# Kernel optimization log

Measured on AMD Instinct MI355X. Metric: run time of the kernel, lower is better.

Reference implementation:

```python
import jax, jax.numpy as jnp
import numpy as np

B, N, D = 4, 4096, 1024
H, DH = 16, 64            # heads, dim_head; inner = H*DH = 1024
FF = 4 * D                # ffn inner dim
EPS = 1e-5


def setup_inputs() -> dict:
    key = jax.random.key(0)
    ks = jax.random.split(key, 8)
    s = 0.02
    return {
        "x": jax.random.normal(ks[0], (B, N, D), jnp.float32),
        "W_qkv": jax.random.normal(ks[1], (D, 3 * H * DH), jnp.float32) * s,
        "W_out": jax.random.normal(ks[2], (H * DH, D), jnp.float32) * s,
        "b_out": jnp.zeros((D,), jnp.float32),
        "ln_g": jnp.ones((D,), jnp.float32),
        "ln_b": jnp.zeros((D,), jnp.float32),
        "W1": jax.random.normal(ks[3], (D, FF), jnp.float32) * s,
        "b1": jnp.zeros((FF,), jnp.float32),
        "W2": jax.random.normal(ks[4], (FF, D), jnp.float32) * s,
        "b2": jnp.zeros((D,), jnp.float32),
    }


def reference(x, W_qkv, W_out, b_out, ln_g, ln_b, W1, b1, W2, b2):
    b, n, _ = x.shape
    scale = DH ** -0.5

    # --- LinearAttention (dual-softmax kernelized attention) ---
    qkv = x @ W_qkv                                   # [b, n, 3*H*DH]
    q, k, v = jnp.split(qkv, 3, axis=-1)
    split = lambda t: t.reshape(b, n, H, DH).transpose(0, 2, 1, 3)  # [b, h, n, d]
    q = jax.nn.softmax(split(q) * scale, axis=-1)     # softmax over head dim
    k = jax.nn.softmax(split(k), axis=-2)             # softmax over sequence
    v = split(v)
    context = jnp.einsum('bhnd,bhne->bhde', q, k)     # [b, h, d, e] -- linear in n
    out = jnp.einsum('bhde,bhnd->bhne', context, v)   # [b, h, n, e]
    out = out.transpose(0, 2, 1, 3).reshape(b, n, H * DH)
    attn = out @ W_out + b_out                        # to_out (dropout=0 at eval)

    # --- LayerNorm ---
    mu = jnp.mean(attn, axis=-1, keepdims=True)
    var = jnp.var(attn, axis=-1, keepdims=True)
    h = (attn - mu) * jax.lax.rsqrt(var + EPS) * ln_g + ln_b

    # --- FeedForward: Linear -> SiLU -> Linear ---
    y = jax.nn.silu(h @ W1 + b1) @ W2 + b2
    return y
```

## Files before the change

### kernel.cpp

```cpp
#include <hip/hip_runtime.h>
#include <hip/hip_bf16.h>

typedef __bf16 bf16x8 __attribute__((ext_vector_type(8)));
typedef __bf16 bf16x4 __attribute__((ext_vector_type(4)));
typedef float  f32x4  __attribute__((ext_vector_type(4)));

#define GLOAD_LDS16(gp, lp) \
  __builtin_amdgcn_global_load_lds((const __attribute__((address_space(1))) void*)(gp), \
                                   (__attribute__((address_space(3))) void*)(lp), 16, 0, 0)


__global__ __launch_bounds__(256) void zero_f32(float* __restrict__ p, int n) {
  int i = (blockIdx.x * 256 + threadIdx.x) * 4;
  if (i < n) *(float4*)(p + i) = make_float4(0.f, 0.f, 0.f, 0.f);
}

__global__ __launch_bounds__(256) void cvt_f32_bf16(const float* __restrict__ in,
                                                    __bf16* __restrict__ out, long n) {
  long i = ((long)blockIdx.x * 256 + threadIdx.x) * 4;
  if (i >= n) return;
  float4 v = *(const float4*)(in + i);
  bf16x4 o;
  o[0] = (__bf16)v.x; o[1] = (__bf16)v.y; o[2] = (__bf16)v.z; o[3] = (__bf16)v.w;
  *(bf16x4*)(out + i) = o;
}

__global__ __launch_bounds__(256) void cvt_wT(const float* __restrict__ W,
                                              __bf16* __restrict__ WT, int K, int N) {
  __shared__ float t[32][33];
  int k0 = blockIdx.x * 32, n0 = blockIdx.y * 32;
  int tx = threadIdx.x, ty = threadIdx.y;
  #pragma unroll
  for (int i = 0; i < 32; i += 8)
    t[ty + i][tx] = W[(size_t)(k0 + ty + i) * N + n0 + tx];
  __syncthreads();
  #pragma unroll
  for (int i = 0; i < 32; i += 8)
    WT[(size_t)(n0 + ty + i) * K + k0 + tx] = (__bf16)t[tx][ty + i];
}


enum { EPI_BF16 = 0, EPI_F32_BIAS = 1, EPI_BF16_SILU = 2, EPI_BF16_BIAS = 3 };

template <int EPI>
__global__ __launch_bounds__(512, 1)
void gemm256(const __bf16* __restrict__ A, const __bf16* __restrict__ B,
             void* __restrict__ Cout, const float* __restrict__ bias,
             int M, int N, int K) {
  __shared__ __bf16 lds[4 * 16384];
  const int tid = threadIdx.x;
  const int w = tid >> 6, l = tid & 63;
  const int brow = blockIdx.x * 256;
  const int bcol = blockIdx.y * 256;
  const int wr = w >> 2, wc = w & 3;
  const int lr = l & 15, lk = (l >> 4) * 8;
  const int rdo = ((lk >> 3) ^ ((lr >> 1) & 3)) << 3;
  const int NT = K >> 5;

  const int rr = w * 16 + (l >> 2);
  const int oct = l & 3;
  const int soct = oct ^ ((rr >> 1) & 3);
  const __bf16* gA0 = A + (size_t)(brow + rr) * K + soct * 8;
  const __bf16* gA1 = A + (size_t)(brow + 128 + rr) * K + soct * 8;
  const __bf16* gB0 = B + (size_t)(bcol + rr) * K + soct * 8;
  const __bf16* gB1 = B + (size_t)(bcol + 128 + rr) * K + soct * 8;
  __bf16* const ldsw = lds + w * 512;

  f32x4 acc[8][4] = {};

  auto stage = [&](int buf) {
    __bf16* d = ldsw + buf * 16384;
    GLOAD_LDS16(gA0, d);
    GLOAD_LDS16(gA1, d + 4096);
    GLOAD_LDS16(gB0, d + 8192);
    GLOAD_LDS16(gB1, d + 12288);
    gA0 += 32; gA1 += 32; gB0 += 32; gB1 += 32;
  };

  stage(0); stage(1); stage(2);

  const int abase = (wr * 128 + lr) * 32 + rdo;
  const int bbase = 8192 + (wc * 64 + lr) * 32 + rdo;

  for (int t = 0; t < NT; ++t) {
    if (t + 2 < NT)      asm volatile("s_waitcnt vmcnt(8)" ::: "memory");
    else if (t + 1 < NT) asm volatile("s_waitcnt vmcnt(4)" ::: "memory");
    else                 asm volatile("s_waitcnt vmcnt(0)" ::: "memory");
    __builtin_amdgcn_s_barrier();
    if (t + 3 < NT) stage((t + 3) & 3);

    const __bf16* sA = lds + (t & 3) * 16384 + abase;
    const __bf16* sB = lds + (t & 3) * 16384 + bbase;

    bf16x8 bfr[4], afr[4];
    #pragma unroll
    for (int n = 0; n < 4; ++n)
      bfr[n] = *(const bf16x8*)(sB + n * 512);
    #pragma unroll
    for (int m = 0; m < 4; ++m)
      afr[m] = *(const bf16x8*)(sA + m * 512);

    __builtin_amdgcn_s_setprio(1);
    #pragma unroll
    for (int m = 0; m < 4; ++m)
      #pragma unroll
      for (int n = 0; n < 4; ++n)
        acc[m][n] = __builtin_amdgcn_mfma_f32_16x16x32_bf16(afr[m], bfr[n], acc[m][n], 0, 0, 0);
    __builtin_amdgcn_s_setprio(0);

    #pragma unroll
    for (int m = 0; m < 4; ++m)
      afr[m] = *(const bf16x8*)(sA + (m + 4) * 512);

    __builtin_amdgcn_s_setprio(1);
    #pragma unroll
    for (int m = 0; m < 4; ++m)
      #pragma unroll
      for (int n = 0; n < 4; ++n)
        acc[m + 4][n] = __builtin_amdgcn_mfma_f32_16x16x32_bf16(afr[m], bfr[n], acc[m + 4][n], 0, 0, 0);
    __builtin_amdgcn_s_setprio(0);
  }

  #pragma unroll
  for (int m = 0; m < 8; ++m) {
    int row0 = brow + wr * 128 + m * 16 + (l >> 4) * 4;
    #pragma unroll
    for (int n = 0; n < 4; ++n) {
      int col = bcol + wc * 64 + n * 16 + lr;
      float bv = (EPI == EPI_BF16) ? 0.f : bias[col];
      #pragma unroll
      for (int j = 0; j < 4; ++j) {
        float v = acc[m][n][j];
        size_t off = (size_t)(row0 + j) * N + col;
        if (EPI == EPI_BF16) {
          ((__bf16*)Cout)[off] = (__bf16)v;
        } else if (EPI == EPI_F32_BIAS) {
          ((float*)Cout)[off] = v + bv;
        } else if (EPI == EPI_BF16_BIAS) {
          ((__bf16*)Cout)[off] = (__bf16)(v + bv);
        } else {
          float z = v + bv;
          ((__bf16*)Cout)[off] = (__bf16)(z / (1.f + __expf(-z)));
        }
      }
    }
  }
}


__global__ __launch_bounds__(256) void q_softmax(__bf16* __restrict__ qkv) {
  qkv += (size_t)blockIdx.z * 4096 * 3072;
  int wg = blockIdx.x * 4 + (threadIdx.x >> 6);
  int l = threadIdx.x & 63;
  int row = wg >> 4, h = wg & 15;
  __bf16* p = qkv + (size_t)row * 3072 + h * 64 + l;
  float v = (float)*p * 0.125f;
  float m = v;
  #pragma unroll
  for (int s = 32; s; s >>= 1) m = fmaxf(m, __shfl_xor(m, s));
  float e = __expf(v - m);
  float sum = e;
  #pragma unroll
  for (int s = 32; s; s >>= 1) sum += __shfl_xor(sum, s);
  *p = (__bf16)(e / sum);
}

__global__ __launch_bounds__(256) void k_exp(__bf16* __restrict__ qkv, float* __restrict__ S) {
  qkv += (size_t)blockIdx.z * 4096 * 3072;
  S   += (size_t)blockIdx.z * 1024;
  int c = blockIdx.x * 256 + threadIdx.x;
  int n0 = blockIdx.y * 128;
  float sum = 0.f;
  __bf16* base = qkv + (size_t)n0 * 3072 + 1024 + c;
  for (int i = 0; i < 128; ++i) {
    __bf16* p = base + (size_t)i * 3072;
    float e = __expf((float)*p);
    __bf16 eb = (__bf16)e;
    *p = eb;
    sum += (float)eb;
  }
  atomicAdd(&S[c], sum);
}

__global__ __launch_bounds__(256) void ctx_gemm(const __bf16* __restrict__ qkv,
                                                float* __restrict__ ctx) {
  qkv += (size_t)blockIdx.z * 4096 * 3072;
  ctx += (size_t)blockIdx.z * 16 * 4096;
  int h = blockIdx.x;
  int k0base = blockIdx.y * 1024;
  __shared__ __bf16 sQ[64 * 32];
  __shared__ __bf16 sK[64 * 32];
  int tid = threadIdx.x, w = tid >> 6, l = tid & 63;
  int lr = l & 15, lk = (l >> 4) * 8;
  int srow = tid >> 3, scol = (tid & 7) * 8;
  f32x4 acc[4] = {};

  for (int kc = 0; kc < 1024; kc += 32) {
    size_t grow = (size_t)(k0base + kc + srow) * 3072;
    bf16x8 qv = *(const bf16x8*)(qkv + grow + h * 64 + scol);
    bf16x8 kv = *(const bf16x8*)(qkv + grow + 1024 + h * 64 + scol);
    __syncthreads();
    #pragma unroll
    for (int j = 0; j < 8; ++j) {
      sQ[(scol + j) * 32 + srow] = qv[j];
      sK[(scol + j) * 32 + srow] = kv[j];
    }
    __syncthreads();
    bf16x8 a = *(const bf16x8*)(sQ + (w * 16 + lr) * 32 + lk);
    #pragma unroll
    for (int n = 0; n < 4; ++n) {
      bf16x8 bb = *(const bf16x8*)(sK + (n * 16 + lr) * 32 + lk);
      acc[n] = __builtin_amdgcn_mfma_f32_16x16x32_bf16(a, bb, acc[n], 0, 0, 0);
    }
  }
  float* cbase = ctx + (size_t)h * 64 * 64;
  #pragma unroll
  for (int n = 0; n < 4; ++n) {
    int col = n * 16 + lr;
    #pragma unroll
    for (int j = 0; j < 4; ++j) {
      int row = w * 16 + (l >> 4) * 4 + j;
      atomicAdd(cbase + row * 64 + col, acc[n][j]);
    }
  }
}

__global__ __launch_bounds__(256) void pv_gemm(const __bf16* __restrict__ qkv,
                                               const float* __restrict__ ctx,
                                               const float* __restrict__ S,
                                               __bf16* __restrict__ outpv) {
  qkv   += (size_t)blockIdx.z * 4096 * 3072;
  ctx   += (size_t)blockIdx.z * 16 * 4096;
  S     += (size_t)blockIdx.z * 1024;
  outpv += (size_t)blockIdx.z * 4096 * 1024;
  int h = blockIdx.y;
  int row0 = blockIdx.x * 128;
  __shared__ __bf16 sC[64 * 64];
  int tid = threadIdx.x;
  const float* cb = ctx + (size_t)h * 4096;
  for (int i = tid; i < 4096; i += 256) {
    int d = i >> 6, e = i & 63;
    sC[e * 64 + d] = (__bf16)cb[i];
  }
  __syncthreads();
  int w = tid >> 6, l = tid & 63;
  int lr = l & 15, lk = (l >> 4) * 8;
  f32x4 acc[2][4] = {};
  const __bf16* vbase = qkv + 2048 + h * 64;
  #pragma unroll
  for (int kk = 0; kk < 64; kk += 32) {
    #pragma unroll
    for (int m = 0; m < 2; ++m) {
      int r = row0 + w * 32 + m * 16 + lr;
      bf16x8 a = *(const bf16x8*)(vbase + (size_t)r * 3072 + kk + lk);
      #pragma unroll
      for (int n = 0; n < 4; ++n) {
        bf16x8 bb = *(const bf16x8*)(sC + (n * 16 + lr) * 64 + kk + lk);
        acc[m][n] = __builtin_amdgcn_mfma_f32_16x16x32_bf16(a, bb, acc[m][n], 0, 0, 0);
      }
    }
  }
  #pragma unroll
  for (int m = 0; m < 2; ++m) {
    int rb = row0 + w * 32 + m * 16 + (l >> 4) * 4;
    #pragma unroll
    for (int n = 0; n < 4; ++n) {
      int e = n * 16 + lr;
      float inv = 1.0f / S[h * 64 + e];
      #pragma unroll
      for (int j = 0; j < 4; ++j)
        outpv[(size_t)(rb + j) * 1024 + h * 64 + e] = (__bf16)(acc[m][n][j] * inv);
    }
  }
}

__global__ __launch_bounds__(256) void layernorm_k(const __bf16* __restrict__ attn,
                                                   const float* __restrict__ g,
                                                   const float* __restrict__ beta,
                                                   __bf16* __restrict__ out) {
  int row = blockIdx.x;
  int t = threadIdx.x;
  bf16x4 v4 = *(const bf16x4*)(attn + (size_t)row * 1024 + t * 4);
  float v0 = (float)v4[0], v1 = (float)v4[1], v2 = (float)v4[2], v3 = (float)v4[3];
  float s = v0 + v1 + v2 + v3;
  float ss = v0 * v0 + v1 * v1 + v2 * v2 + v3 * v3;
  #pragma unroll
  for (int sh = 32; sh; sh >>= 1) { s += __shfl_xor(s, sh); ss += __shfl_xor(ss, sh); }
  __shared__ float red[8];
  int w = t >> 6, l = t & 63;
  if (l == 0) { red[w] = s; red[4 + w] = ss; }
  __syncthreads();
  s = red[0] + red[1] + red[2] + red[3];
  ss = red[4] + red[5] + red[6] + red[7];
  float mu = s * (1.f / 1024.f);
  float var = ss * (1.f / 1024.f) - mu * mu;
  float rstd = rsqrtf(var + 1e-5f);
  float4 gg = *(const float4*)(g + t * 4);
  float4 bb = *(const float4*)(beta + t * 4);
  bf16x4 o;
  o[0] = (__bf16)((v0 - mu) * rstd * gg.x + bb.x);
  o[1] = (__bf16)((v1 - mu) * rstd * gg.y + bb.y);
  o[2] = (__bf16)((v2 - mu) * rstd * gg.z + bb.z);
  o[3] = (__bf16)((v3 - mu) * rstd * gg.w + bb.w);
  *(bf16x4*)(out + (size_t)row * 1024 + t * 4) = o;
}


extern "C" void kernel_launch(void* const* d_in, const int* in_sizes, int n_in,
                              void* d_out, int out_size, void* d_ws, size_t ws_size,
                              hipStream_t stream) {
  const float* x     = (const float*)d_in[0];
  const float* W_qkv = (const float*)d_in[1];
  const float* W_out = (const float*)d_in[2];
  const float* b_out = (const float*)d_in[3];
  const float* ln_g  = (const float*)d_in[4];
  const float* ln_b  = (const float*)d_in[5];
  const float* W1    = (const float*)d_in[6];
  const float* b1    = (const float*)d_in[7];
  const float* W2    = (const float*)d_in[8];
  const float* b2    = (const float*)d_in[9];

  char* ws = (char*)d_ws;
  size_t off = 0;
  auto alloc = [&](size_t bytes) { void* p = ws + off; off += (bytes + 255) & ~(size_t)255; return p; };

  __bf16* wqkvT = (__bf16*)alloc(3072ull * 1024 * 2);
  __bf16* woutT = (__bf16*)alloc(1024ull * 1024 * 2);
  __bf16* w1T   = (__bf16*)alloc(4096ull * 1024 * 2);
  __bf16* w2T   = (__bf16*)alloc(1024ull * 4096 * 2);

  cvt_wT<<<dim3(32, 96), dim3(32, 8), 0, stream>>>(W_qkv, wqkvT, 1024, 3072);
  cvt_wT<<<dim3(32, 32), dim3(32, 8), 0, stream>>>(W_out, woutT, 1024, 1024);
  cvt_wT<<<dim3(32, 128), dim3(32, 8), 0, stream>>>(W1, w1T, 1024, 4096);
  cvt_wT<<<dim3(128, 32), dim3(32, 8), 0, stream>>>(W2, w2T, 4096, 1024);

  const size_t FULL_NEED = 196ull << 20;

  if (ws_size >= FULL_NEED) {
    float*  Sctx  = (float*)alloc((4096ull + 4 * 16 * 4096) * 4);
    __bf16* xb    = (__bf16*)alloc(16384ull * 1024 * 2);
    __bf16* qkv   = (__bf16*)alloc(16384ull * 3072 * 2);
    __bf16* outpv = (__bf16*)alloc(16384ull * 1024 * 2);

    float* S   = Sctx;
    float* ctx = Sctx + 4096;
    __bf16* attn = (__bf16*)((char*)qkv + (64ull << 20));
    __bf16* hln  = xb;
    __bf16* ffn1 = qkv;

    cvt_f32_bf16<<<16384, 256, 0, stream>>>(x, xb, 16777216L);
    zero_f32<<<260, 256, 0, stream>>>(Sctx, 266240);

    gemm256<EPI_BF16><<<dim3(64, 12), 512, 0, stream>>>(xb, wqkvT, qkv, nullptr, 16384, 3072, 1024);
    q_softmax<<<dim3(16384, 1, 4), 256, 0, stream>>>(qkv);
    k_exp<<<dim3(4, 32, 4), 256, 0, stream>>>(qkv, S);
    ctx_gemm<<<dim3(16, 4, 4), 256, 0, stream>>>(qkv, ctx);
    pv_gemm<<<dim3(32, 16, 4), 256, 0, stream>>>(qkv, ctx, S, outpv);

    gemm256<EPI_BF16_BIAS><<<dim3(64, 4), 512, 0, stream>>>(outpv, woutT, attn, b_out, 16384, 1024, 1024);
    layernorm_k<<<16384, 256, 0, stream>>>(attn, ln_g, ln_b, hln);
    gemm256<EPI_BF16_SILU><<<dim3(64, 16), 512, 0, stream>>>(hln, w1T, ffn1, b1, 16384, 4096, 1024);
    gemm256<EPI_F32_BIAS><<<dim3(64, 4), 512, 0, stream>>>(ffn1, w2T, (float*)d_out, b2, 16384, 1024, 4096);
  } else {
    float*  Sctx  = (float*)alloc(66560ull * 4);
    __bf16* xb    = (__bf16*)alloc(16384ull * 1024 * 2);
    __bf16* outpv = (__bf16*)alloc(16384ull * 1024 * 2);
    __bf16* qkv_b = (__bf16*)alloc(4096ull * 3072 * 2);

    float* S   = Sctx;
    float* ctx = Sctx + 1024;
    __bf16* attn = xb;
    __bf16* hln  = outpv;
    __bf16* fchunk = xb;

    cvt_f32_bf16<<<16384, 256, 0, stream>>>(x, xb, 16777216L);

    for (int b = 0; b < 4; ++b) {
      const __bf16* xb_b = xb + (size_t)b * 4096 * 1024;
      gemm256<EPI_BF16><<<dim3(16, 12), 512, 0, stream>>>(xb_b, wqkvT, qkv_b, nullptr, 4096, 3072, 1024);
      zero_f32<<<65, 256, 0, stream>>>(Sctx, 66560);
      q_softmax<<<dim3(16384, 1, 1), 256, 0, stream>>>(qkv_b);
      k_exp<<<dim3(4, 32, 1), 256, 0, stream>>>(qkv_b, S);
      ctx_gemm<<<dim3(16, 4, 1), 256, 0, stream>>>(qkv_b, ctx);
      pv_gemm<<<dim3(32, 16, 1), 256, 0, stream>>>(qkv_b, ctx, S, outpv + (size_t)b * 4096 * 1024);
    }

    gemm256<EPI_BF16_BIAS><<<dim3(64, 4), 512, 0, stream>>>(outpv, woutT, attn, b_out, 16384, 1024, 1024);
    layernorm_k<<<16384, 256, 0, stream>>>(attn, ln_g, ln_b, hln);

    for (int c = 0; c < 4; ++c) {
      const __bf16* h_c = hln + (size_t)c * 4096 * 1024;
      float* out_c = (float*)d_out + (size_t)c * 4096 * 1024;
      gemm256<EPI_BF16_SILU><<<dim3(16, 16), 512, 0, stream>>>(h_c, w1T, fchunk, b1, 4096, 4096, 1024);
      gemm256<EPI_F32_BIAS><<<dim3(16, 4), 512, 0, stream>>>(fchunk, w2T, out_c, b2, 4096, 1024, 4096);
    }
  }
}
```

Before: 587.5 us.

## Restructure GEMM main loop into 64-wide K tiles with interleaved half-stage prefetch

Replaces the 4-buffer, 32-wide-K ring in the 256x256 GEMM with two 64-wide K buffers, each split into two 32-wide halves. Each iteration runs four sub-phases, and each sub-phase issues the prefetch for one A or B half between its LDS reads and its MFMA block. It adds explicit lgkmcnt waits with scheduling barriers. The aim is to spread global-to-LDS traffic evenly across the MFMA work and cut the number of full barrier-wait points per K element. The cost is more barriers per iteration and tighter hand-managed vmcnt accounting, which is fragile.

```diff
diff --git a/kernel.cpp b/kernel.cpp
--- a/kernel.cpp
+++ b/kernel.cpp
@@ -8,6 +8,8 @@
 #define GLOAD_LDS16(gp, lp) \
   __builtin_amdgcn_global_load_lds((const __attribute__((address_space(1))) void*)(gp), \
                                    (__attribute__((address_space(3))) void*)(lp), 16, 0, 0)
+#define LGKM0 do { asm volatile("s_waitcnt lgkmcnt(0)" ::: "memory"); \
+                   __builtin_amdgcn_sched_barrier(0); } while (0)
 
 
 __global__ __launch_bounds__(256) void zero_f32(float* __restrict__ p, int n) {
@@ -47,78 +49,123 @@
 void gemm256(const __bf16* __restrict__ A, const __bf16* __restrict__ B,
              void* __restrict__ Cout, const float* __restrict__ bias,
              int M, int N, int K) {
-  __shared__ __bf16 lds[4 * 16384];
+  __shared__ __bf16 lds[65536];
   const int tid = threadIdx.x;
   const int w = tid >> 6, l = tid & 63;
   const int brow = blockIdx.x * 256;
   const int bcol = blockIdx.y * 256;
   const int wr = w >> 2, wc = w & 3;
-  const int lr = l & 15, lk = (l >> 4) * 8;
-  const int rdo = ((lk >> 3) ^ ((lr >> 1) & 3)) << 3;
-  const int NT = K >> 5;
-
-  const int rr = w * 16 + (l >> 2);
-  const int oct = l & 3;
-  const int soct = oct ^ ((rr >> 1) & 3);
-  const __bf16* gA0 = A + (size_t)(brow + rr) * K + soct * 8;
-  const __bf16* gA1 = A + (size_t)(brow + 128 + rr) * K + soct * 8;
-  const __bf16* gB0 = B + (size_t)(bcol + rr) * K + soct * 8;
-  const __bf16* gB1 = B + (size_t)(bcol + 128 + rr) * K + soct * 8;
-  __bf16* const ldsw = lds + w * 512;
+  const int lr = l & 15;
+  const int rdo8 = ((l >> 4) ^ ((lr >> 1) & 3)) << 3;
+  const int NT = K >> 6;
+
+  const int aoff = (wr * 128 + lr) * 32 + rdo8;
+  const int boff = 16384 + (wc * 64 + lr) * 32 + rdo8;
+
+  const int srow = w * 16 + (l >> 2);
+  const int soct8 = ((l & 3) ^ ((l >> 3) & 3)) * 8;
+  const __bf16* pA0 = A + (size_t)(brow + srow) * K + soct8;
+  const __bf16* pA1 = A + (size_t)(brow + 128 + srow) * K + soct8;
+  const __bf16* pB0 = B + (size_t)(bcol + srow) * K + soct8;
+  const __bf16* pB1 = B + (size_t)(bcol + 128 + srow) * K + soct8;
+
+  auto stageA = [&](int k, int Tt) {
+    size_t cofs = (size_t)Tt * 64 + k * 32;
+    __bf16* d = lds + (Tt & 1) * 32768 + k * 8192 + w * 512;
+    GLOAD_LDS16(pA0 + cofs, d);
+    GLOAD_LDS16(pA1 + cofs, d + 4096);
+  };
+  auto stageB = [&](int k, int Tt) {
+    size_t cofs = (size_t)Tt * 64 + k * 32;
+    __bf16* d = lds + (Tt & 1) * 32768 + 16384 + k * 8192 + w * 512;
+    GLOAD_LDS16(pB0 + cofs, d);
+    GLOAD_LDS16(pB1 + cofs, d + 4096);
+  };
 
   f32x4 acc[8][4] = {};
-
-  auto stage = [&](int buf) {
-    __bf16* d = ldsw + buf * 16384;
-    GLOAD_LDS16(gA0, d);
-    GLOAD_LDS16(gA1, d + 4096);
-    GLOAD_LDS16(gB0, d + 8192);
-    GLOAD_LDS16(gB1, d + 12288);
-    gA0 += 32; gA1 += 32; gB0 += 32; gB1 += 32;
-  };
-
-  stage(0); stage(1); stage(2);
-
-  const int abase = (wr * 128 + lr) * 32 + rdo;
-  const int bbase = 8192 + (wc * 64 + lr) * 32 + rdo;
-
-  for (int t = 0; t < NT; ++t) {
-    if (t + 2 < NT)      asm volatile("s_waitcnt vmcnt(8)" ::: "memory");
-    else if (t + 1 < NT) asm volatile("s_waitcnt vmcnt(4)" ::: "memory");
-    else                 asm volatile("s_waitcnt vmcnt(0)" ::: "memory");
+  bf16x8 afr[4], bfr[4];
+
+  stageA(0, 0); stageB(0, 0);
+  stageA(1, 0); stageB(1, 0);
+  stageA(0, 1); stageB(0, 1);
+
+  for (int T = 0; T < NT; ++T) {
+    const int buf = (T & 1) * 32768;
+    const bool s1 = (T + 1 < NT), s2 = (T + 2 < NT);
+
+    if (s1) asm volatile("s_waitcnt vmcnt(8)" ::: "memory");
+    else    asm volatile("s_waitcnt vmcnt(4)" ::: "memory");
     __builtin_amdgcn_s_barrier();
-    if (t + 3 < NT) stage((t + 3) & 3);
-
-    const __bf16* sA = lds + (t & 3) * 16384 + abase;
-    const __bf16* sB = lds + (t & 3) * 16384 + bbase;
-
-    bf16x8 bfr[4], afr[4];
-    #pragma unroll
-    for (int n = 0; n < 4; ++n)
-      bfr[n] = *(const bf16x8*)(sB + n * 512);
-    #pragma unroll
-    for (int m = 0; m < 4; ++m)
-      afr[m] = *(const bf16x8*)(sA + m * 512);
-
-    __builtin_amdgcn_s_setprio(1);
-    #pragma unroll
-    for (int m = 0; m < 4; ++m)
-      #pragma unroll
-      for (int n = 0; n < 4; ++n)
-        acc[m][n] = __builtin_amdgcn_mfma_f32_16x16x32_bf16(afr[m], bfr[n], acc[m][n], 0, 0, 0);
-    __builtin_amdgcn_s_setprio(0);
-
-    #pragma unroll
-    for (int m = 0; m < 4; ++m)
-      afr[m] = *(const bf16x8*)(sA + (m + 4) * 512);
-
-    __builtin_amdgcn_s_setprio(1);
-    #pragma unroll
-    for (int m = 0; m < 4; ++m)
-      #pragma unroll
-      for (int n = 0; n < 4; ++n)
-        acc[m + 4][n] = __builtin_amdgcn_mfma_f32_16x16x32_bf16(afr[m], bfr[n], acc[m + 4][n], 0, 0, 0);
-    __builtin_amdgcn_s_setprio(0);
+    {
+      const __bf16* pb = lds + buf + boff;
+      const __bf16* pa = lds + buf + aoff;
+      #pragma unroll
+      for (int n = 0; n < 4; ++n) bfr[n] = *(const bf16x8*)(pb + n * 512);
+      #pragma unroll
+      for (int m = 0; m < 4; ++m) afr[m] = *(const bf16x8*)(pa + m * 512);
+      if (s1) stageA(1, T + 1);
+      LGKM0;
+      __builtin_amdgcn_s_setprio(1);
+      #pragma unroll
+      for (int m = 0; m < 4; ++m)
+        #pragma unroll
+        for (int n = 0; n < 4; ++n)
+          acc[m][n] = __builtin_amdgcn_mfma_f32_16x16x32_bf16(afr[m], bfr[n], acc[m][n], 0, 0, 0);
+      __builtin_amdgcn_s_setprio(0);
+    }
+
+    __builtin_amdgcn_s_barrier();
+    {
+      const __bf16* pa = lds + buf + aoff + 2048;
+      #pragma unroll
+      for (int m = 0; m < 4; ++m) afr[m] = *(const bf16x8*)(pa + m * 512);
+      if (s1) stageB(1, T + 1);
+      LGKM0;
+      __builtin_amdgcn_s_setprio(1);
+      #pragma unroll
+      for (int m = 0; m < 4; ++m)
+        #pragma unroll
+        for (int n = 0; n < 4; ++n)
+          acc[m + 4][n] = __builtin_amdgcn_mfma_f32_16x16x32_bf16(afr[m], bfr[n], acc[m + 4][n], 0, 0, 0);
+      __builtin_amdgcn_s_setprio(0);
+    }
+
+    if (s1) asm volatile("s_waitcnt vmcnt(8)" ::: "memory");
+    else    asm volatile("s_waitcnt vmcnt(0)" ::: "memory");
+    __builtin_amdgcn_s_barrier();
+    {
+      const __bf16* pb = lds + buf + 8192 + boff;
+      const __bf16* pa = lds + buf + 8192 + aoff;
+      #pragma unroll
+      for (int n = 0; n < 4; ++n) bfr[n] = *(const bf16x8*)(pb + n * 512);
+      #pragma unroll
+      for (int m = 0; m < 4; ++m) afr[m] = *(const bf16x8*)(pa + m * 512);
+      if (s2) stageA(0, T + 2);
+      LGKM0;
+      __builtin_amdgcn_s_setprio(1);
+      #pragma unroll
+      for (int m = 0; m < 4; ++m)
+        #pragma unroll
+        for (int n = 0; n < 4; ++n)
+          acc[m][n] = __builtin_amdgcn_mfma_f32_16x16x32_bf16(afr[m], bfr[n], acc[m][n], 0, 0, 0);
+      __builtin_amdgcn_s_setprio(0);
+    }
+
+    __builtin_amdgcn_s_barrier();
+    {
+      const __bf16* pa = lds + buf + 8192 + aoff + 2048;
+      #pragma unroll
+      for (int m = 0; m < 4; ++m) afr[m] = *(const bf16x8*)(pa + m * 512);
+      if (s2) stageB(0, T + 2);
+      LGKM0;
+      __builtin_amdgcn_s_setprio(1);
+      #pragma unroll
+      for (int m = 0; m < 4; ++m)
+        #pragma unroll
+        for (int n = 0; n < 4; ++n)
+          acc[m + 4][n] = __builtin_amdgcn_mfma_f32_16x16x32_bf16(afr[m], bfr[n], acc[m + 4][n], 0, 0, 0);
+      __builtin_amdgcn_s_setprio(0);
+    }
   }
 
   #pragma unroll
```

Measured after the change: 583.3 us, median of 2. About the same (-0.7%).
